# Kernel optimization log

Hardware: AMD Instinct MI355X
Metric: run time of the kernel (lower is better)

The kernel has to match this reference:

```python
import jax, jax.numpy as jnp
import numpy as np

L, B, S, E, N = 4, 1, 2048, 768, 12
H = E // N
FF = 4 * E
EPS = 1e-5


def setup_inputs() -> dict:
    key = jax.random.key(0)
    ks = jax.random.split(key, 12)
    g = lambda i, shape, sc=0.02: jax.random.normal(ks[i], shape, jnp.float32) * sc
    return {
        "x": jax.random.normal(ks[0], (B, S, E), jnp.float32),
        "mask": jnp.tril(jnp.ones((1, 1, S, S), jnp.int32)),  # causal
        "c_attn_w": g(1, (L, E, 3 * E)),
        "c_attn_b": g(2, (L, 3 * E)),
        "c_proj_w": g(3, (L, E, E)),
        "c_proj_b": g(4, (L, E)),
        "ln1_w": jnp.ones((L, E), jnp.float32),
        "ln1_b": jnp.zeros((L, E), jnp.float32),
        "fc_w": g(5, (L, E, FF)),
        "fc_b": g(6, (L, FF)),
        "proj_w": g(7, (L, FF, E)),
        "proj_b": g(8, (L, E)),
        "ln2_w": jnp.ones((L, E), jnp.float32),
        "ln2_b": jnp.zeros((L, E), jnp.float32),
        "lnf_w": jnp.ones((E,), jnp.float32),
        "lnf_b": jnp.zeros((E,), jnp.float32),
    }


def _layer_norm(x, w, b):
    m = jnp.mean(x, axis=-1, keepdims=True)
    v = jnp.mean(jnp.square(x - m), axis=-1, keepdims=True)
    return (x - m) * jax.lax.rsqrt(v + EPS) * w + b


def reference(x, mask, c_attn_w, c_attn_b, c_proj_w, c_proj_b,
              ln1_w, ln1_b, fc_w, fc_b, proj_w, proj_b,
              ln2_w, ln2_b, lnf_w, lnf_b):
    masked = (mask == 0)  # [1,1,S,S] bool, True where attention is disallowed
    # cf_ composes right-to-left: Decoder applies final LayerNorm FIRST,
    # then blocks in reversed list order (scan reverse=True), dropout=identity (eval).
    h0 = _layer_norm(x, lnf_w, lnf_b)

    def block(h, p):
        Wqkv, bqkv, Wp, bp, w1, b1, Wf, bf, Wo, bo, w2, b2 = p
        qkv = h @ Wqkv + bqkv                      # [B,S,3E]
        q, k, v = jnp.split(qkv, 3, axis=-1)
        hd = lambda t: t.reshape(B, S, N, H).transpose(0, 2, 1, 3)  # [B,N,S,H]
        q, k, v = hd(q), hd(k), hd(v)
        att = jnp.einsum('bnsh,bnth->bnst', q, k) / jnp.sqrt(jnp.float32(H))
        att = jnp.where(masked, -jnp.inf, att)
        att = jax.nn.softmax(att, axis=-1)         # [B,N,S,S]
        y = jnp.einsum('bnst,bnth->bnsh', att, v)  # [B,N,S,H]
        y = y.transpose(0, 2, 1, 3).reshape(B, S, E) @ Wp + bp
        h = _layer_norm(y + h, w1, b1)             # post-norm residual 1
        m = jax.nn.gelu(h @ Wf + bf, approximate=False) @ Wo + bo
        h = _layer_norm(m + h, w2, b2)             # post-norm residual 2
        return h, None

    out, _ = jax.lax.scan(
        block, h0,
        (c_attn_w, c_attn_b, c_proj_w, c_proj_b, ln1_w, ln1_b,
         fc_w, fc_b, proj_w, proj_b, ln2_w, ln2_b),
        reverse=True)
    return out
```

## Files before the change

kernel.cpp:

```cpp
#include <hip/hip_runtime.h>
#include <hip/hip_bf16.h>
#include <math.h>

#define S_LEN 2048
#define E_DIM 768
#define NHEAD 12
#define FF_DIM 3072
#define L_LAYERS 4

typedef __attribute__((ext_vector_type(8))) short short8;
typedef __attribute__((ext_vector_type(4))) float f32x4;
typedef __attribute__((ext_vector_type(4))) unsigned short ushort4_t;
typedef __attribute__((ext_vector_type(2))) unsigned int uint2v;

__device__ __forceinline__ unsigned short f2bf(float f) {
  union { float f; unsigned u; } v; v.f = f;
  unsigned r = v.u + 0x7fffu + ((v.u >> 16) & 1u);
  return (unsigned short)(r >> 16);
}

__device__ __forceinline__ unsigned cvtpk(float lo, float hi) {
  unsigned r;
  asm("v_cvt_pk_bf16_f32 %0, %1, %2" : "=v"(r) : "v"(lo), "v"(hi));
  return r;
}

__device__ __forceinline__ f32x4 MFMA(short8 a, short8 b, f32x4 c) {
  return __builtin_amdgcn_mfma_f32_16x16x32_bf16(a, b, c, 0, 0, 0);
}

__device__ __forceinline__ void gld_lds16(const void* g, void* l) {
  __builtin_amdgcn_global_load_lds(
      (const __attribute__((address_space(1))) void*)g,
      (__attribute__((address_space(3))) void*)l, 16, 0, 0);
}

__global__ __launch_bounds__(256)
void transpose_cast(const float* __restrict__ src, short* __restrict__ dst,
                    int K, int Nn) {
  __shared__ float tile[32][33];
  src += (size_t)blockIdx.z * K * Nn;
  dst += (size_t)blockIdx.z * K * Nn;
  const int i0 = blockIdx.x * 32;
  const int j0 = blockIdx.y * 32;
  const int tx = threadIdx.x & 31, ty = threadIdx.x >> 5;
#pragma unroll
  for (int r = 0; r < 32; r += 8)
    tile[ty + r][tx] = src[(size_t)(i0 + ty + r) * Nn + j0 + tx];
  __syncthreads();
#pragma unroll
  for (int r = 0; r < 32; r += 8)
    dst[(size_t)(j0 + ty + r) * K + i0 + tx] = (short)f2bf(tile[tx][ty + r]);
}

__global__ __launch_bounds__(256)
void ln_kernel(const float* __restrict__ parts, int P,
               const float* __restrict__ b2, const float* __restrict__ colBias,
               const float* __restrict__ w, const float* __restrict__ bb,
               float* __restrict__ outF, short* __restrict__ outB) {
  const int row = blockIdx.x;
  const int t = threadIdx.x;
  __shared__ float red[4], red2[4];
  float v[3];
  const size_t plane = (size_t)S_LEN * E_DIM;
#pragma unroll
  for (int i = 0; i < 3; ++i) {
    const int c = t + i * 256;
    float acc = colBias ? colBias[c] : 0.f;
    if (b2) acc += b2[(size_t)row * E_DIM + c];
    for (int p = 0; p < P; ++p)
      acc += parts[p * plane + (size_t)row * E_DIM + c];
    v[i] = acc;
  }
  float s = v[0] + v[1] + v[2];
#pragma unroll
  for (int off = 32; off; off >>= 1) s += __shfl_down(s, off);
  const int ln = t & 63, wv = t >> 6;
  if (ln == 0) red[wv] = s;
  __syncthreads();
  const float mean = (red[0] + red[1] + red[2] + red[3]) * (1.0f / E_DIM);
  float qs = 0.f;
#pragma unroll
  for (int i = 0; i < 3; ++i) { float d = v[i] - mean; qs += d * d; }
#pragma unroll
  for (int off = 32; off; off >>= 1) qs += __shfl_down(qs, off);
  if (ln == 0) red2[wv] = qs;
  __syncthreads();
  const float var = (red2[0] + red2[1] + red2[2] + red2[3]) * (1.0f / E_DIM);
  const float rs = rsqrtf(var + 1e-5f);
#pragma unroll
  for (int i = 0; i < 3; ++i) {
    const int c = t + i * 256;
    float o = (v[i] - mean) * rs * w[c] + bb[c];
    outF[(size_t)row * E_DIM + c] = o;
    outB[(size_t)row * E_DIM + c] = (short)f2bf(o);
  }
}

template <int EPI>
__global__ __launch_bounds__(256)
void gemm_nt(const short* __restrict__ A, const short* __restrict__ Bt,
             const float* __restrict__ bias, float* __restrict__ outF,
             short* __restrict__ outB, short* __restrict__ qOut,
             short* __restrict__ kOut, short* __restrict__ vtOut,
             int M, int Nn, int K, int kLen) {
  __shared__ alignas(16) short As[64 * 32];
  __shared__ alignas(16) short Bs[128 * 32];
  const int bm = blockIdx.x, bn = blockIdx.y;
  const int t = threadIdx.x;
  const int ln = t & 63, wv = t >> 6;
  const int wr = wv >> 1, wc = wv & 1;
  const int lr = ln & 15, lg = ln >> 4;
  f32x4 acc[2][4] = {};

  const int kStart = blockIdx.z * kLen;
  const int kEnd = kStart + kLen;
  const int srow = wv * 16 + (ln >> 2);
  const int scol = (ln & 3) * 8;
  const short* Abase = A + (size_t)bm * 64 * K;
  const short* Bbase = Bt + (size_t)bn * 128 * K;

  for (int k0 = kStart; k0 < kEnd; k0 += 32) {
    if (k0 != kStart) __syncthreads();
    gld_lds16(Abase + (size_t)srow * K + k0 + scol, As + wv * 512);
#pragma unroll
    for (int half = 0; half < 2; ++half)
      gld_lds16(Bbase + (size_t)(half * 64 + srow) * K + k0 + scol,
                Bs + half * 2048 + wv * 512);
    __syncthreads();
    short8 af[2], bfr[4];
#pragma unroll
    for (int m = 0; m < 2; ++m)
      af[m] = *(const short8*)(As + (wr * 32 + m * 16 + lr) * 32 + lg * 8);
#pragma unroll
    for (int n = 0; n < 4; ++n)
      bfr[n] = *(const short8*)(Bs + (wc * 64 + n * 16 + lr) * 32 + lg * 8);
#pragma unroll
    for (int m = 0; m < 2; ++m)
#pragma unroll
      for (int n = 0; n < 4; ++n)
        acc[m][n] = MFMA(af[m], bfr[n], acc[m][n]);
  }

  if constexpr (EPI == 0) outF += (size_t)blockIdx.z * ((size_t)M * Nn);

#pragma unroll
  for (int m = 0; m < 2; ++m) {
#pragma unroll
    for (int n = 0; n < 4; ++n) {
      const int colb = bn * 128 + wc * 64 + n * 16;
      const int row0 = bm * 64 + wr * 32 + m * 16 + lg * 4;
      if constexpr (EPI == 0) {
#pragma unroll
        for (int r = 0; r < 4; ++r)
          outF[(size_t)(row0 + r) * Nn + colb + lr] = acc[m][n][r];
      } else if constexpr (EPI == 1) {
#pragma unroll
        for (int r = 0; r < 4; ++r) {
          float vv = acc[m][n][r] + bias[colb + lr];
          float g = 0.5f * vv * (1.0f + erff(vv * 0.70710678118f));
          outB[(size_t)(row0 + r) * Nn + colb + lr] = (short)f2bf(g);
        }
      } else {
        float vv[4];
#pragma unroll
        for (int r = 0; r < 4; ++r) vv[r] = acc[m][n][r] + bias[colb + lr];
        const int which = colb / E_DIM;
        const int wcolb = colb - which * E_DIM;
        const int head = wcolb >> 6;
        const int hh = (wcolb & 63) + lr;
        if (which == 2) {
          ushort4_t pk;
#pragma unroll
          for (int r = 0; r < 4; ++r) pk[r] = f2bf(vv[r]);
          *(ushort4_t*)(vtOut + ((size_t)head * 64 + hh) * S_LEN + row0) = pk;
        } else if (which == 0) {
#pragma unroll
          for (int r = 0; r < 4; ++r)
            qOut[((size_t)head * S_LEN + row0 + r) * 64 + hh] =
                (short)f2bf(vv[r] * 0.125f);
        } else {
#pragma unroll
          for (int r = 0; r < 4; ++r)
            kOut[((size_t)head * S_LEN + row0 + r) * 64 + hh] =
                (short)f2bf(vv[r]);
        }
      }
    }
  }
}

__global__ __launch_bounds__(256)
void attn_kernel(const short* __restrict__ q, const short* __restrict__ k,
                 const short* __restrict__ vt, short* __restrict__ y,
                 float* __restrict__ pO, float* __restrict__ pML) {
  __shared__ alignas(16) short KS[2][64 * 64];
  __shared__ alignas(16) short VS[2][64 * 64];
  __shared__ alignas(16) short P[4][16 * 64];
  const int bx = blockIdx.x;
  int head, qt, tile0, ntl, mode;
  bool hasDiag;
  if (bx < 192) {
    head = bx % NHEAD; qt = 31 - bx / NHEAD;
    tile0 = 0; ntl = 16; hasDiag = false; mode = 1;
  } else if (bx < 384) {
    const int b = bx - 192;
    head = b % NHEAD; qt = 31 - b / NHEAD;
    tile0 = 16; ntl = qt + 1 - 16; hasDiag = true; mode = 2;
  } else {
    const int b = bx - 384;
    head = b % NHEAD; qt = 15 - b / NHEAD;
    tile0 = 0; ntl = qt + 1; hasDiag = true; mode = 0;
  }
  const int qb = qt * 64;
  const int t = threadIdx.x;
  const int ln = t & 63, wv = t >> 6;
  const int lr = ln & 15, lg = ln >> 4;
  const int l7 = lr & 7;

  const int srow = ln >> 3;
  const int sg = (ln & 7) ^ srow;
  const short* kbase = k + (size_t)head * S_LEN * 64;
  const short* vbase = vt + (size_t)head * 64 * S_LEN;

  auto stage = [&](int buf, int t0) {
#pragma unroll
    for (int i = 0; i < 2; ++i) {
      const int c = wv * 2 + i;
      gld_lds16(kbase + (size_t)(t0 + c * 8 + srow) * 64 + sg * 8,
                &KS[buf][c * 512]);
      gld_lds16(vbase + (size_t)(c * 8 + srow) * S_LEN + t0 + sg * 8,
                &VS[buf][c * 512]);
    }
  };

  short8 qa[2];
  {
    const short* qp =
        q + ((size_t)head * S_LEN + qb + wv * 16 + lr) * 64 + lg * 8;
    qa[0] = *(const short8*)qp;
    qa[1] = *(const short8*)(qp + 32);
  }

  f32x4 o[4] = {};
  float mrun = -1e30f, lrun = 0.f;

  stage(0, tile0 * 64);
  for (int i = 0; i < ntl; ++i) {
    __syncthreads();
    if (i + 1 < ntl) stage((i + 1) & 1, (tile0 + i + 1) * 64);
    const short* KSb = KS[i & 1];
    const short* VSb = VS[i & 1];
    const int t0 = (tile0 + i) * 64;

    f32x4 sc[4];
#pragma unroll
    for (int cc = 0; cc < 4; ++cc) {
      f32x4 z = {};
#pragma unroll
      for (int kk = 0; kk < 2; ++kk)
        z = MFMA(*(const short8*)(KSb + (cc * 16 + lr) * 64 +
                                  (((kk * 4 + lg) ^ l7) * 8)),
                 qa[kk], z);
      sc[cc] = z;
    }

    if (hasDiag && i == ntl - 1) {
      const int qg = qb + wv * 16 + lr;
#pragma unroll
      for (int cc = 0; cc < 4; ++cc)
#pragma unroll
        for (int r = 0; r < 4; ++r)
          if (t0 + cc * 16 + lg * 4 + r > qg) sc[cc][r] = -1e30f;
    }

    float mx = sc[0][0];
#pragma unroll
    for (int cc = 0; cc < 4; ++cc)
#pragma unroll
      for (int r = 0; r < 4; ++r) mx = fmaxf(mx, sc[cc][r]);
    mx = fmaxf(mx, __shfl_xor(mx, 16));
    mx = fmaxf(mx, __shfl_xor(mx, 32));
    const unsigned long long an = __ballot(mx > mrun);
    float fsc = 1.f;
    if (an) {
      const float mn = fmaxf(mrun, mx);
      fsc = __expf(mrun - mn);
      mrun = mn;
    }

    float ss = 0.f;
    unsigned pk[8];
#pragma unroll
    for (int cc = 0; cc < 4; ++cc) {
      const float p0 = __expf(sc[cc][0] - mrun);
      const float p1 = __expf(sc[cc][1] - mrun);
      const float p2 = __expf(sc[cc][2] - mrun);
      const float p3 = __expf(sc[cc][3] - mrun);
      ss += (p0 + p1) + (p2 + p3);
      pk[2 * cc] = cvtpk(p0, p1);
      pk[2 * cc + 1] = cvtpk(p2, p3);
    }
    ss += __shfl_xor(ss, 16);
    ss += __shfl_xor(ss, 32);
    lrun = lrun * fsc + ss;

#pragma unroll
    for (int cc = 0; cc < 4; ++cc) {
      uint2v w2; w2.x = pk[2 * cc]; w2.y = pk[2 * cc + 1];
      *(uint2v*)(&P[wv][lr * 64 + (((cc * 2 + (lg >> 1)) ^ l7) * 8) +
                        (lg & 1) * 4]) = w2;
    }

    if (an) {
      float fr[4];
#pragma unroll
      for (int r = 0; r < 4; ++r) fr[r] = __shfl(fsc, lg * 4 + r);
#pragma unroll
      for (int n = 0; n < 4; ++n)
#pragma unroll
        for (int r = 0; r < 4; ++r) o[n][r] *= fr[r];
    }

    short8 pa[2];
#pragma unroll
    for (int kk = 0; kk < 2; ++kk)
      pa[kk] = *(const short8*)(&P[wv][lr * 64 + (((kk * 4 + lg) ^ l7) * 8)]);
#pragma unroll
    for (int n = 0; n < 4; ++n)
#pragma unroll
      for (int kk = 0; kk < 2; ++kk)
        o[n] = MFMA(pa[kk],
                    *(const short8*)(VSb + (n * 16 + lr) * 64 +
                                     (((kk * 4 + lg) ^ l7) * 8)),
                    o[n]);
  }

  if (mode == 0) {
    float inv[4];
#pragma unroll
    for (int r = 0; r < 4; ++r) inv[r] = 1.0f / __shfl(lrun, lg * 4 + r);
#pragma unroll
    for (int n = 0; n < 4; ++n)
#pragma unroll
      for (int r = 0; r < 4; ++r)
        y[(size_t)(qb + wv * 16 + lg * 4 + r) * E_DIM + head * 64 + n * 16 +
          lr] = (short)f2bf(o[n][r] * inv[r]);
  } else {
    const int p = (qt - 16) * NHEAD + head;
    float* ob = pO + ((size_t)(mode - 1) * 192 + p) * 4096;
#pragma unroll
    for (int n = 0; n < 4; ++n)
#pragma unroll
      for (int r = 0; r < 4; ++r)
        ob[(wv * 16 + lg * 4 + r) * 64 + n * 16 + lr] = o[n][r];
    float* mlb = pML + ((size_t)(mode - 1) * 192 + p) * 128;
    if (lg == 0) {
      mlb[wv * 16 + lr] = mrun;
      mlb[64 + wv * 16 + lr] = lrun;
    }
  }
}

__global__ __launch_bounds__(256)
void attn_merge(const float* __restrict__ pO, const float* __restrict__ pML,
                short* __restrict__ y) {
  const int p = blockIdx.x;
  const int qt = 16 + p / NHEAD, head = p % NHEAD;
  const int t = threadIdx.x;
  const int hd = t & 63, q0 = t >> 6;
  const float* o1 = pO + (size_t)p * 4096;
  const float* o2 = pO + (size_t)(192 + p) * 4096;
  const float* ml1 = pML + (size_t)p * 128;
  const float* ml2 = pML + (size_t)(192 + p) * 128;
#pragma unroll
  for (int i = 0; i < 16; ++i) {
    const int qq = q0 + i * 4;
    const float m1 = ml1[qq], l1 = ml1[64 + qq];
    const float m2 = ml2[qq], l2 = ml2[64 + qq];
    const float M = fmaxf(m1, m2);
    const float w1 = __expf(m1 - M), w2 = __expf(m2 - M);
    const float val =
        (o1[qq * 64 + hd] * w1 + o2[qq * 64 + hd] * w2) / (l1 * w1 + l2 * w2);
    y[(size_t)(qt * 64 + qq) * E_DIM + head * 64 + hd] = (short)f2bf(val);
  }
}

extern "C" void kernel_launch(void* const* d_in, const int* in_sizes, int n_in,
                              void* d_out, int out_size, void* d_ws,
                              size_t ws_size, hipStream_t stream) {
  const float* x       = (const float*)d_in[0];
  const float* attn_w  = (const float*)d_in[2];
  const float* attn_b  = (const float*)d_in[3];
  const float* cproj_w = (const float*)d_in[4];
  const float* cproj_b = (const float*)d_in[5];
  const float* ln1_w   = (const float*)d_in[6];
  const float* ln1_b   = (const float*)d_in[7];
  const float* fc_w    = (const float*)d_in[8];
  const float* fc_b    = (const float*)d_in[9];
  const float* proj_w  = (const float*)d_in[10];
  const float* proj_b  = (const float*)d_in[11];
  const float* ln2_w   = (const float*)d_in[12];
  const float* ln2_b   = (const float*)d_in[13];
  const float* lnf_w   = (const float*)d_in[14];
  const float* lnf_b   = (const float*)d_in[15];

  char* ws = (char*)d_ws;
  size_t off = 0;
  auto alloc = [&](size_t bytes) {
    char* p = ws + off;
    off += (bytes + 255) & ~(size_t)255;
    return p;
  };
  short* attnT = (short*)alloc((size_t)L_LAYERS * E_DIM * 3 * E_DIM * 2);
  short* projT = (short*)alloc((size_t)L_LAYERS * E_DIM * E_DIM * 2);
  short* fcT   = (short*)alloc((size_t)L_LAYERS * E_DIM * FF_DIM * 2);
  short* p2T   = (short*)alloc((size_t)L_LAYERS * FF_DIM * E_DIM * 2);
  float* hF    = (float*)alloc((size_t)S_LEN * E_DIM * 4);
  short* hB    = (short*)alloc((size_t)S_LEN * E_DIM * 2);
  short* qB    = (short*)alloc((size_t)NHEAD * S_LEN * 64 * 2);
  short* kB    = (short*)alloc((size_t)NHEAD * S_LEN * 64 * 2);
  short* vT    = (short*)alloc((size_t)NHEAD * S_LEN * 64 * 2);
  short* yB    = (short*)alloc((size_t)S_LEN * E_DIM * 2);
  short* aB    = (short*)alloc((size_t)S_LEN * FF_DIM * 2);
  float* partF = (float*)alloc((size_t)4 * S_LEN * E_DIM * 4);
  float* pO  = partF;
  float* pML = partF + 2 * 192 * 4096;

  transpose_cast<<<dim3(E_DIM / 32, 3 * E_DIM / 32, L_LAYERS), 256, 0, stream>>>(
      attn_w, attnT, E_DIM, 3 * E_DIM);
  transpose_cast<<<dim3(E_DIM / 32, E_DIM / 32, L_LAYERS), 256, 0, stream>>>(
      cproj_w, projT, E_DIM, E_DIM);
  transpose_cast<<<dim3(E_DIM / 32, FF_DIM / 32, L_LAYERS), 256, 0, stream>>>(
      fc_w, fcT, E_DIM, FF_DIM);
  transpose_cast<<<dim3(FF_DIM / 32, E_DIM / 32, L_LAYERS), 256, 0, stream>>>(
      proj_w, p2T, FF_DIM, E_DIM);

  ln_kernel<<<S_LEN, 256, 0, stream>>>(x, 1, nullptr, nullptr, lnf_w, lnf_b,
                                       hF, hB);

  for (int l = L_LAYERS - 1; l >= 0; --l) {
    gemm_nt<2><<<dim3(S_LEN / 64, 3 * E_DIM / 128, 1), 256, 0, stream>>>(
        hB, attnT + (size_t)l * E_DIM * 3 * E_DIM,
        attn_b + (size_t)l * 3 * E_DIM, nullptr, nullptr, qB, kB, vT,
        S_LEN, 3 * E_DIM, E_DIM, E_DIM);
    attn_kernel<<<dim3(576), 256, 0, stream>>>(qB, kB, vT, yB, pO, pML);
    attn_merge<<<dim3(192), 256, 0, stream>>>(pO, pML, yB);
    gemm_nt<0><<<dim3(S_LEN / 64, E_DIM / 128, 3), 256, 0, stream>>>(
        yB, projT + (size_t)l * E_DIM * E_DIM, nullptr,
        partF, nullptr, nullptr, nullptr, nullptr, S_LEN, E_DIM, E_DIM, 256);
    ln_kernel<<<S_LEN, 256, 0, stream>>>(partF, 3, hF,
                                         cproj_b + (size_t)l * E_DIM,
                                         ln1_w + (size_t)l * E_DIM,
                                         ln1_b + (size_t)l * E_DIM, hF, hB);
    gemm_nt<1><<<dim3(S_LEN / 64, FF_DIM / 128, 1), 256, 0, stream>>>(
        hB, fcT + (size_t)l * E_DIM * FF_DIM, fc_b + (size_t)l * FF_DIM,
        nullptr, aB, nullptr, nullptr, nullptr, S_LEN, FF_DIM, E_DIM, E_DIM);
    gemm_nt<0><<<dim3(S_LEN / 64, E_DIM / 128, 4), 256, 0, stream>>>(
        aB, p2T + (size_t)l * FF_DIM * E_DIM, nullptr,
        partF, nullptr, nullptr, nullptr, nullptr, S_LEN, E_DIM, FF_DIM, 768);
    float* outTarget = (l == 0) ? (float*)d_out : hF;
    ln_kernel<<<S_LEN, 256, 0, stream>>>(partF, 4, hF,
                                         proj_b + (size_t)l * E_DIM,
                                         ln2_w + (size_t)l * E_DIM,
                                         ln2_b + (size_t)l * E_DIM, outTarget,
                                         hB);
  }
}
```

Before: 506.7 us.

## Double-buffer GEMM LDS tiles with K=64 steps and XOR-swizzled layout

The shared GEMM kernel now uses two LDS buffers, so the global-to-LDS load for the next K slice is issued while MFMAs run on the current one. The K step grows from 32 to 64, and the LDS layout is XOR-swizzled so fragment reads avoid bank conflicts. This halves the barriers per unit of K and hides load latency. In exchange, LDS use per block rises to 48KB, which may reduce occupancy, and kLen must now be a multiple of 64.

```diff
diff --git a/kernel.cpp b/kernel.cpp
--- a/kernel.cpp
+++ b/kernel.cpp
@@ -104,42 +104,63 @@
              short* __restrict__ outB, short* __restrict__ qOut,
              short* __restrict__ kOut, short* __restrict__ vtOut,
              int M, int Nn, int K, int kLen) {
-  __shared__ alignas(16) short As[64 * 32];
-  __shared__ alignas(16) short Bs[128 * 32];
+  __shared__ alignas(16) short As[2][64 * 64];
+  __shared__ alignas(16) short Bs[2][128 * 64];
   const int bm = blockIdx.x, bn = blockIdx.y;
   const int t = threadIdx.x;
   const int ln = t & 63, wv = t >> 6;
   const int wr = wv >> 1, wc = wv & 1;
   const int lr = ln & 15, lg = ln >> 4;
+  const int l7 = lr & 7;
   f32x4 acc[2][4] = {};
 
   const int kStart = blockIdx.z * kLen;
-  const int kEnd = kStart + kLen;
-  const int srow = wv * 16 + (ln >> 2);
-  const int scol = (ln & 3) * 8;
-  const short* Abase = A + (size_t)bm * 64 * K;
-  const short* Bbase = Bt + (size_t)bn * 128 * K;
-
-  for (int k0 = kStart; k0 < kEnd; k0 += 32) {
-    if (k0 != kStart) __syncthreads();
-    gld_lds16(Abase + (size_t)srow * K + k0 + scol, As + wv * 512);
-#pragma unroll
-    for (int half = 0; half < 2; ++half)
-      gld_lds16(Bbase + (size_t)(half * 64 + srow) * K + k0 + scol,
-                Bs + half * 2048 + wv * 512);
+  const int nSteps = kLen / 64;
+  const int srow = ln >> 3;
+  const int sg = (ln & 7) ^ srow;
+  const short* Abase = A + (size_t)bm * 64 * K + kStart + sg * 8;
+  const short* Bbase = Bt + (size_t)bn * 128 * K + kStart + sg * 8;
+
+  auto stage = [&](int buf, int ko) {
+#pragma unroll
+    for (int i = 0; i < 2; ++i) {
+      const int c = wv * 2 + i;
+      gld_lds16(Abase + (size_t)(c * 8 + srow) * K + ko, &As[buf][c * 512]);
+    }
+#pragma unroll
+    for (int i = 0; i < 4; ++i) {
+      const int c = wv * 4 + i;
+      gld_lds16(Bbase + (size_t)(c * 8 + srow) * K + ko, &Bs[buf][c * 512]);
+    }
+  };
+
+  stage(0, 0);
+  __syncthreads();
+  int cur = 0;
+  for (int s = 0; s < nSteps; ++s) {
+    if (s + 1 < nSteps) stage(cur ^ 1, (s + 1) * 64);
+    short8 af[2][2], bfr[4][2];
+#pragma unroll
+    for (int m = 0; m < 2; ++m)
+#pragma unroll
+      for (int kk = 0; kk < 2; ++kk)
+        af[m][kk] = *(const short8*)(&As[cur][(wr * 32 + m * 16 + lr) * 64 +
+                                             (((kk * 4 + lg) ^ l7) * 8)]);
+#pragma unroll
+    for (int n = 0; n < 4; ++n)
+#pragma unroll
+      for (int kk = 0; kk < 2; ++kk)
+        bfr[n][kk] = *(const short8*)(&Bs[cur][(wc * 64 + n * 16 + lr) * 64 +
+                                              (((kk * 4 + lg) ^ l7) * 8)]);
+#pragma unroll
+    for (int m = 0; m < 2; ++m)
+#pragma unroll
+      for (int n = 0; n < 4; ++n)
+#pragma unroll
+        for (int kk = 0; kk < 2; ++kk)
+          acc[m][n] = MFMA(af[m][kk], bfr[n][kk], acc[m][n]);
     __syncthreads();
-    short8 af[2], bfr[4];
-#pragma unroll
-    for (int m = 0; m < 2; ++m)
-      af[m] = *(const short8*)(As + (wr * 32 + m * 16 + lr) * 32 + lg * 8);
-#pragma unroll
-    for (int n = 0; n < 4; ++n)
-      bfr[n] = *(const short8*)(Bs + (wc * 64 + n * 16 + lr) * 32 + lg * 8);
-#pragma unroll
-    for (int m = 0; m < 2; ++m)
-#pragma unroll
-      for (int n = 0; n < 4; ++n)
-        acc[m][n] = MFMA(af[m], bfr[n], acc[m][n]);
+    cur ^= 1;
   }
 
   if constexpr (EPI == 0) outF += (size_t)blockIdx.z * ((size_t)M * Nn);
```

Result: faster. 460.4 us (-9.1%).
